# Performance work log

Hardware: AMD Instinct MI355X
Metric: run time of the kernel (lower is better)

## Reference

```python
import jax, jax.numpy as jnp
import numpy as np

N_NODES = 50000
N_EDGES = 1600000
IN_FEAT = 128
OUT_FEAT = 128


def setup_inputs() -> dict:
    key = jax.random.key(0)
    k_x, k_w, k_v, k_r, k_c = jax.random.split(key, 5)
    X = jax.random.normal(k_x, (N_NODES, IN_FEAT), dtype=jnp.float32)
    # nn.Linear(in_feat, out_feat, bias=False) weight: [out_feat, in_feat]
    W = jax.random.normal(k_w, (OUT_FEAT, IN_FEAT), dtype=jnp.float32) * (1.0 / np.sqrt(IN_FEAT))
    # Sparse adjacency A in COO form: A[rows[e], cols[e]] = vals[e]
    A_vals = jax.random.uniform(k_v, (N_EDGES,), dtype=jnp.float32)
    A_rows = jax.random.randint(k_r, (N_EDGES,), 0, N_NODES, dtype=jnp.int32)
    A_cols = jax.random.randint(k_c, (N_EDGES,), 0, N_NODES, dtype=jnp.int32)
    return {"X": X, "W": W, "A_vals": A_vals, "A_rows": A_rows, "A_cols": A_cols}


def reference(X, W, A_vals, A_rows, A_cols):
    # H = linear(X) = X @ W.T  -> [N, out_feat]
    H = jnp.einsum("ni,oi->no", X, W)
    # out = A @ H via COO SpMM: gather source rows, scale by edge value,
    # scatter-add into destination rows.
    msgs = A_vals[:, None] * H[A_cols]            # [E, out_feat]
    out = jax.ops.segment_sum(msgs, A_rows, num_segments=N_NODES)
    return out
```

## Files before the change

kernel.cpp:

```cpp
#include <hip/hip_runtime.h>


constexpr int N_NODES = 50000;
constexpr int N_EDGES = 1600000;
constexpr int FEAT    = 128;

constexpr int ROWS_PER_BIN = 64;
constexpr int NB           = (N_NODES + ROWS_PER_BIN - 1) / ROWS_PER_BIN;
constexpr int CAP          = 2560;
constexpr int CHUNK        = 4096;
constexpr int EPT          = 4;
constexpr int PART_BLOCKS  = (N_EDGES + CHUNK - 1) / CHUNK;
constexpr int GEMM_BLOCKS  = (N_NODES + 255) / 256;
constexpr int FUSED_GROUPS = 196;
constexpr int FUSED_BLOCKS = FUSED_GROUPS * 3;
constexpr int OVF_CAP      = 8192;

constexpr int RSLOT    = 64;
constexpr int ROVF_CAP = 256;

static_assert(NB % 2 == 0, "bin<->block mapping needs even NB");

constexpr int PITCH = 136;

typedef short short8 __attribute__((ext_vector_type(8)));
typedef float f32x4  __attribute__((ext_vector_type(4)));
typedef float f32x2  __attribute__((ext_vector_type(2)));

__device__ __forceinline__ unsigned short f2bf(float x) {
    unsigned u = __float_as_uint(x);
    u += 0x7fffu + ((u >> 16) & 1u);
    return (unsigned short)(u >> 16);
}
__device__ __forceinline__ float bf2f(unsigned short s) {
    return __uint_as_float(((unsigned)s) << 16);
}

__device__ __forceinline__ float dec_val10(unsigned w) {
    return (float)(w & 1023u) * (1.0f / 1023.0f);
}

__device__ void gemm_body(const float* __restrict__ X, const float* __restrict__ W,
                          unsigned short* __restrict__ Hb, int g,
                          unsigned short* Wsh) {
    const int tid  = threadIdx.x;
    const int row0 = g * 256;

#pragma unroll
    for (int t = 0; t < 4; t++) {
        int idx = tid + 1024 * t;
        int r   = idx >> 5;
        int c4  = (idx & 31) << 2;
        const float4 v = *(const float4*)&W[r * FEAT + c4];
        unsigned lo = f2bf(v.x) | ((unsigned)f2bf(v.y) << 16);
        unsigned hi = f2bf(v.z) | ((unsigned)f2bf(v.w) << 16);
        *(uint2*)&Wsh[r * PITCH + c4] = make_uint2(lo, hi);
    }
    __syncthreads();

    const int w    = tid >> 6;
    const int lane = tid & 63;
    const int n    = lane & 15;
    const int q    = lane >> 4;

    f32x4 acc[8];
#pragma unroll
    for (int t = 0; t < 8; t++) acc[t] = (f32x4){0.f, 0.f, 0.f, 0.f};

    int xrow = row0 + 16 * w + n;
    if (xrow >= N_NODES) xrow = N_NODES - 1;
    const float* xp = X + (size_t)xrow * FEAT;

#pragma unroll
    for (int kt = 0; kt < 4; kt++) {
        const int ko = kt * 32 + q * 8;
        const float4 a0 = *(const float4*)&xp[ko];
        const float4 a1 = *(const float4*)&xp[ko + 4];
        short8 bfrag;
        bfrag[0] = (short)f2bf(a0.x); bfrag[1] = (short)f2bf(a0.y);
        bfrag[2] = (short)f2bf(a0.z); bfrag[3] = (short)f2bf(a0.w);
        bfrag[4] = (short)f2bf(a1.x); bfrag[5] = (short)f2bf(a1.y);
        bfrag[6] = (short)f2bf(a1.z); bfrag[7] = (short)f2bf(a1.w);
#pragma unroll
        for (int t = 0; t < 8; t++) {
            const short8 afrag = *(const short8*)&Wsh[(16 * t + n) * PITCH + ko];
            acc[t] = __builtin_amdgcn_mfma_f32_16x16x32_bf16(afrag, bfrag, acc[t], 0, 0, 0);
        }
    }

    const int grow = row0 + 16 * w + n;
    if (grow < N_NODES) {
#pragma unroll
        for (int t = 0; t < 8; t++) {
            ushort4 pk;
            pk.x = f2bf(acc[t][0]); pk.y = f2bf(acc[t][1]);
            pk.z = f2bf(acc[t][2]); pk.w = f2bf(acc[t][3]);
            const int col0 = 16 * t + 4 * q;
            unsigned short* dst = Hb + ((size_t)(col0 >> 5) * N_NODES + grow) * 32
                                     + (col0 & 31);
            *(ushort4*)dst = pk;
        }
    }
}

__device__ void partition_body(const int* __restrict__ rows, const int* __restrict__ cols,
                               const float* __restrict__ vals,
                               int* __restrict__ gcur, unsigned* __restrict__ binbuf,
                               int* __restrict__ ovf_cnt, int* __restrict__ ovf,
                               int g, int* smem) {
    int* hist  = smem;
    int* wbase = smem + NB;
    const int tid = threadIdx.x;
    const int e0  = g * CHUNK;

    for (int i = tid; i < NB; i += 1024) hist[i] = 0;
    __syncthreads();

    int      myrow[EPT], myrank[EPT];
    unsigned myword[EPT];
#pragma unroll
    for (int t = 0; t < EPT; t++) {
        int e = e0 + t * 1024 + tid;
        if (e < N_EDGES) {
            int r = rows[e];
            unsigned vq = (unsigned)__float2int_rn(vals[e] * 1023.0f);
            myrow[t]  = r;
            myword[t] = ((unsigned)(r & 63) << 26) | ((unsigned)cols[e] << 10) | vq;
            myrank[t] = atomicAdd(&hist[r >> 6], 1);
        } else {
            myrow[t] = -1; myword[t] = 0; myrank[t] = 0;
        }
    }
    __syncthreads();

    for (int i = tid; i < NB; i += 1024) {
        int c = hist[i];
        wbase[i] = (c > 0) ? atomicAdd(&gcur[i], c) : 0;
    }
    __syncthreads();

#pragma unroll
    for (int t = 0; t < EPT; t++) {
        int r = myrow[t];
        if (r < 0) continue;
        int b    = r >> 6;
        int rank = wbase[b] + myrank[t];
        if (rank < CAP) {
            binbuf[(size_t)b * CAP + rank] = myword[t];
        } else {
            int k = atomicAdd(ovf_cnt, 1);
            if (k < OVF_CAP) ovf[k] = e0 + t * 1024 + tid;
        }
    }
}

__global__ __launch_bounds__(1024) void gemm_partition(
    const float* __restrict__ X, const float* __restrict__ W,
    unsigned short* __restrict__ Hb,
    const int* __restrict__ rows, const int* __restrict__ cols,
    const float* __restrict__ vals,
    int* __restrict__ gcur, unsigned* __restrict__ binbuf,
    int* __restrict__ ovf_cnt, int* __restrict__ ovf) {
    __shared__ unsigned short Wsh[128 * PITCH];
    const int grp = blockIdx.x / 3;
    const int rem = blockIdx.x - grp * 3;
    if (rem == 2) {
        gemm_body(X, W, Hb, grp, Wsh);
    } else {
        int pg = grp * 2 + rem;
        if (pg < PART_BLOCKS)
            partition_body(rows, cols, vals, gcur, binbuf, ovf_cnt, ovf, pg, (int*)Wsh);
    }
}

__global__ __launch_bounds__(512) void spmm_bins(
    const int* __restrict__ gcur, const unsigned* __restrict__ binbuf,
    const unsigned short* __restrict__ Hb, float* __restrict__ out,
    const int* __restrict__ rows, const int* __restrict__ cols,
    const float* __restrict__ vals,
    const int* __restrict__ ovf_cnt, const int* __restrict__ ovf) {
    __shared__ unsigned sorted[ROWS_PER_BIN * RSLOT];
    __shared__ int cur[ROWS_PER_BIN];
    __shared__ unsigned rovf[ROVF_CAP];
    __shared__ int rovf_cnt;

    const int bid  = blockIdx.x;
    const int q    = (bid & 7) >> 1;
    const int b    = (bid >> 3) * 2 + (bid & 1);
    const int tid  = threadIdx.x;
    const int lane = tid & 63;
    const int w    = tid >> 6;

    if (tid < ROWS_PER_BIN) cur[tid] = 0;
    if (tid == ROWS_PER_BIN) rovf_cnt = 0;
    __syncthreads();

    int cnt = gcur[b];
    if (cnt > CAP) cnt = CAP;
    const unsigned* bb = binbuf + (size_t)b * CAP;

    for (int i = tid; i < cnt; i += 512) {
        unsigned m   = bb[i];
        int rl       = (int)(m >> 26);
        int pos      = atomicAdd(&cur[rl], 1);
        unsigned col = (m >> 10) & 0xffffu;
        unsigned vb  = (unsigned)f2bf(dec_val10(m));
        if (pos < RSLOT) {
            sorted[rl * RSLOT + pos] = (vb << 16) | col;
        } else {
            int k = atomicAdd(&rovf_cnt, 1);
            if (k < ROVF_CAP) rovf[k] = m;
        }
    }
    __syncthreads();

    int nrovf = rovf_cnt;
    if (nrovf > ROVF_CAP) nrovf = ROVF_CAP;
    int novf = *ovf_cnt;
    if (novf > OVF_CAP) novf = OVF_CAP;

    const int row0   = b * ROWS_PER_BIN;
    const int slot   = lane >> 4;
    const int lane16 = lane & 15;
    const ushort2* __restrict__ Hq2 = (const ushort2*)(Hb + (size_t)q * N_NODES * 32);
    float2* out2 = (float2*)out;

    for (int rr = 0; rr < 8; rr++) {
        const int rl = w * 8 + rr;
        const int gr = row0 + rl;
        if (gr >= N_NODES) break;
        int e = cur[rl];
        if (e > RSLOT) e = RSLOT;
        const unsigned* srow = &sorted[rl * RSLOT];

        float accx = 0.f, accy = 0.f;
        int i = 0;
        for (; i + 16 <= e; i += 16) {
            float   vv[4];
            ushort2 hh[4];
#pragma unroll
            for (int u = 0; u < 4; u++) {
                unsigned m = srow[i + u * 4 + slot];
                vv[u] = __uint_as_float(m & 0xffff0000u);
                hh[u] = Hq2[(int)(m & 0xffffu) * 16 + lane16];
            }
#pragma unroll
            for (int u = 0; u < 4; u++) {
                accx += vv[u] * bf2f(hh[u].x);
                accy += vv[u] * bf2f(hh[u].y);
            }
        }
        for (; i < e; i += 4) {
            int idx = i + slot;
            unsigned m = (idx < e) ? srow[idx] : 0u;
            float v2 = __uint_as_float(m & 0xffff0000u);
            ushort2 h2 = Hq2[(int)(m & 0xffffu) * 16 + lane16];
            accx += v2 * bf2f(h2.x);
            accy += v2 * bf2f(h2.y);
        }
        for (int k = 0; k < nrovf; k++) {
            unsigned m = rovf[k];
            if ((int)(m >> 26) == rl && slot == 0) {
                float vv = dec_val10(m);
                ushort2 h2 = Hq2[(int)((m >> 10) & 0xffffu) * 16 + lane16];
                accx += vv * bf2f(h2.x);
                accy += vv * bf2f(h2.y);
            }
        }
        for (int k = 0; k < novf; k++) {
            int e2 = ovf[k];
            if (rows[e2] == gr && slot == 0) {
                float vv = vals[e2];
                ushort2 h2 = Hq2[cols[e2] * 16 + lane16];
                accx += vv * bf2f(h2.x);
                accy += vv * bf2f(h2.y);
            }
        }
        accx += __shfl_xor(accx, 16); accy += __shfl_xor(accy, 16);
        accx += __shfl_xor(accx, 32); accy += __shfl_xor(accy, 32);
        if (slot == 0) {
            f32x2 r; r[0] = accx; r[1] = accy;
            __builtin_nontemporal_store(r, (f32x2*)&out2[(size_t)gr * 64 + q * 16 + lane16]);
        }
    }
}

__global__ __launch_bounds__(1024) void gemm_only(
    const float* __restrict__ X, const float* __restrict__ W,
    unsigned short* __restrict__ Hb) {
    __shared__ unsigned short Wsh[128 * PITCH];
    gemm_body(X, W, Hb, blockIdx.x, Wsh);
}

__global__ __launch_bounds__(256) void spmm_push_atomic(
    const int* __restrict__ rows, const int* __restrict__ cols,
    const float* __restrict__ vals, const unsigned short* __restrict__ Hb,
    float* __restrict__ out) {
    const int e    = blockIdx.x * 4 + (threadIdx.x >> 6);
    const int lane = threadIdx.x & 63;
    if (e >= N_EDGES) return;
    int r = rows[e], c = cols[e];
    float v = vals[e];
    const int f1 = lane, f2 = lane + 64;
    float h1 = bf2f(Hb[((size_t)(f1 >> 5) * N_NODES + c) * 32 + (f1 & 31)]);
    float h2 = bf2f(Hb[((size_t)(f2 >> 5) * N_NODES + c) * 32 + (f2 & 31)]);
    atomicAdd(&out[r * FEAT + f1], v * h1);
    atomicAdd(&out[r * FEAT + f2], v * h2);
}

extern "C" void kernel_launch(void* const* d_in, const int* in_sizes, int n_in,
                              void* d_out, int out_size, void* d_ws, size_t ws_size,
                              hipStream_t stream) {
    const float* X      = (const float*)d_in[0];
    const float* W      = (const float*)d_in[1];
    const float* A_vals = (const float*)d_in[2];
    const int*   A_rows = (const int*)d_in[3];
    const int*   A_cols = (const int*)d_in[4];
    float* out = (float*)d_out;

    auto align256 = [](size_t x) { return (x + 255) & ~size_t(255); };
    char* ws = (char*)d_ws;

    size_t off = 0;
    size_t hb_off   = off; off += align256(size_t(N_NODES) * FEAT * 2);
    size_t gcur_off = off; off += align256(size_t(NB) * sizeof(int));
    size_t ovfc_off = off; off += 256;
    size_t ovf_off  = off; off += align256(size_t(OVF_CAP) * sizeof(int));
    size_t bin_off  = off; off += size_t(NB) * CAP * sizeof(unsigned);
    const size_t need = off;

    unsigned short* Hb = (unsigned short*)(ws + hb_off);

    if (ws_size >= need) {
        int*      gcur    = (int*)(ws + gcur_off);
        int*      ovf_cnt = (int*)(ws + ovfc_off);
        int*      ovf     = (int*)(ws + ovf_off);
        unsigned* binbuf  = (unsigned*)(ws + bin_off);

        (void)hipMemsetAsync(ws + gcur_off, 0, (ovfc_off - gcur_off) + 256, stream);
        gemm_partition<<<FUSED_BLOCKS, 1024, 0, stream>>>(X, W, Hb, A_rows, A_cols, A_vals,
                                                          gcur, binbuf, ovf_cnt, ovf);
        spmm_bins<<<NB * 4, 512, 0, stream>>>(gcur, binbuf, Hb, out,
                                              A_rows, A_cols, A_vals, ovf_cnt, ovf);
    } else {
        gemm_only<<<GEMM_BLOCKS, 1024, 0, stream>>>(X, W, Hb);
        (void)hipMemsetAsync(out, 0, size_t(N_NODES) * FEAT * sizeof(float), stream);
        spmm_push_atomic<<<(N_EDGES + 3) / 4, 256, 0, stream>>>(A_rows, A_cols, A_vals, Hb, out);
    }
}
```

Measured before the change: 164.2 us.

## Replace bin partitioning with per-row slot buckets and row-wise SpMM gather

```diff
diff --git a/kernel.cpp b/kernel.cpp
--- a/kernel.cpp
+++ b/kernel.cpp
@@ -16,6 +16,7 @@
 constexpr int FUSED_BLOCKS = FUSED_GROUPS * 3;
 constexpr int OVF_CAP      = 8192;
 
+constexpr int RSLOT_G  = 64;
 constexpr int RSLOT    = 64;
 constexpr int ROVF_CAP = 256;
 
@@ -35,7 +36,6 @@
 __device__ __forceinline__ float bf2f(unsigned short s) {
     return __uint_as_float(((unsigned)s) << 16);
 }
-
 __device__ __forceinline__ float dec_val10(unsigned w) {
     return (float)(w & 1023u) * (1.0f / 1023.0f);
 }
@@ -99,6 +99,121 @@
             unsigned short* dst = Hb + ((size_t)(col0 >> 5) * N_NODES + grow) * 32
                                      + (col0 & 31);
             *(ushort4*)dst = pk;
+        }
+    }
+}
+
+__device__ void partition_v2_body(const int* __restrict__ rows, const int* __restrict__ cols,
+                                  const float* __restrict__ vals,
+                                  int* __restrict__ rowcnt, unsigned* __restrict__ rowbuf,
+                                  int* __restrict__ ovf_cnt, int* __restrict__ ovf, int g) {
+    const int tid = threadIdx.x;
+    const int e0  = g * CHUNK;
+#pragma unroll
+    for (int t = 0; t < EPT; t++) {
+        int e = e0 + t * 1024 + tid;
+        if (e >= N_EDGES) continue;
+        int r = rows[e];
+        int c = cols[e];
+        int vq = __float2int_rn(vals[e] * 1023.0f);
+        unsigned vb = (unsigned)f2bf((float)vq * (1.0f / 1023.0f));
+        int pos = atomicAdd(&rowcnt[r], 1);
+        if (pos < RSLOT_G) {
+            rowbuf[(size_t)r * RSLOT_G + pos] = (vb << 16) | (unsigned)c;
+        } else {
+            int k = atomicAdd(ovf_cnt, 1);
+            if (k < OVF_CAP) ovf[k] = e;
+        }
+    }
+}
+
+__global__ __launch_bounds__(1024) void gemm_partition_v2(
+    const float* __restrict__ X, const float* __restrict__ W,
+    unsigned short* __restrict__ Hb,
+    const int* __restrict__ rows, const int* __restrict__ cols,
+    const float* __restrict__ vals,
+    int* __restrict__ rowcnt, unsigned* __restrict__ rowbuf,
+    int* __restrict__ ovf_cnt, int* __restrict__ ovf) {
+    __shared__ unsigned short Wsh[128 * PITCH];
+    const int grp = blockIdx.x / 3;
+    const int rem = blockIdx.x - grp * 3;
+    if (rem == 2) {
+        gemm_body(X, W, Hb, grp, Wsh);
+    } else {
+        int pg = grp * 2 + rem;
+        if (pg < PART_BLOCKS)
+            partition_v2_body(rows, cols, vals, rowcnt, rowbuf, ovf_cnt, ovf, pg);
+    }
+}
+
+__global__ __launch_bounds__(512) void spmm_rows(
+    const int* __restrict__ rowcnt, const unsigned* __restrict__ rowbuf,
+    const unsigned short* __restrict__ Hb, float* __restrict__ out,
+    const int* __restrict__ rows, const int* __restrict__ cols,
+    const float* __restrict__ vals,
+    const int* __restrict__ ovf_cnt, const int* __restrict__ ovf) {
+    const int bid  = blockIdx.x;
+    const int q    = (bid & 7) >> 1;
+    const int b    = (bid >> 3) * 2 + (bid & 1);
+    const int tid  = threadIdx.x;
+    const int lane = tid & 63;
+    const int w    = tid >> 6;
+
+    const int slot   = lane >> 4;
+    const int lane16 = lane & 15;
+    const ushort2* __restrict__ Hq2 = (const ushort2*)(Hb + (size_t)q * N_NODES * 32);
+    float2* out2 = (float2*)out;
+
+    int novf = *ovf_cnt;
+    if (novf > OVF_CAP) novf = OVF_CAP;
+
+    const int row0 = b * ROWS_PER_BIN;
+    for (int rr = 0; rr < 8; rr++) {
+        const int gr = row0 + w * 8 + rr;
+        if (gr >= N_NODES) break;
+        int e = rowcnt[gr];
+        if (e > RSLOT_G) e = RSLOT_G;
+        const unsigned* __restrict__ srow = rowbuf + (size_t)gr * RSLOT_G;
+
+        float accx = 0.f, accy = 0.f;
+        int i = 0;
+        for (; i + 16 <= e; i += 16) {
+            float   vv[4];
+            ushort2 hh[4];
+#pragma unroll
+            for (int u = 0; u < 4; u++) {
+                unsigned m = srow[i + u * 4 + slot];
+                vv[u] = __uint_as_float(m & 0xffff0000u);
+                hh[u] = Hq2[(int)(m & 0xffffu) * 16 + lane16];
+            }
+#pragma unroll
+            for (int u = 0; u < 4; u++) {
+                accx += vv[u] * bf2f(hh[u].x);
+                accy += vv[u] * bf2f(hh[u].y);
+            }
+        }
+        for (; i < e; i += 4) {
+            int idx = i + slot;
+            unsigned m = (idx < e) ? srow[idx] : 0u;
+            float v2 = __uint_as_float(m & 0xffff0000u);
+            ushort2 h2 = Hq2[(int)(m & 0xffffu) * 16 + lane16];
+            accx += v2 * bf2f(h2.x);
+            accy += v2 * bf2f(h2.y);
+        }
+        for (int k = 0; k < novf; k++) {
+            int e2 = ovf[k];
+            if (rows[e2] == gr && slot == 0) {
+                float vv = vals[e2];
+                ushort2 h2 = Hq2[cols[e2] * 16 + lane16];
+                accx += vv * bf2f(h2.x);
+                accy += vv * bf2f(h2.y);
+            }
+        }
+        accx += __shfl_xor(accx, 16); accy += __shfl_xor(accy, 16);
+        accx += __shfl_xor(accx, 32); accy += __shfl_xor(accy, 32);
+        if (slot == 0) {
+            f32x2 r; r[0] = accx; r[1] = accy;
+            __builtin_nontemporal_store(r, (f32x2*)&out2[(size_t)gr * 64 + q * 16 + lane16]);
         }
     }
 }
@@ -323,21 +438,39 @@
 
     size_t off = 0;
     size_t hb_off   = off; off += align256(size_t(N_NODES) * FEAT * 2);
-    size_t gcur_off = off; off += align256(size_t(NB) * sizeof(int));
+    size_t rc_off   = off; off += align256(size_t(N_NODES) * sizeof(int));
     size_t ovfc_off = off; off += 256;
     size_t ovf_off  = off; off += align256(size_t(OVF_CAP) * sizeof(int));
-    size_t bin_off  = off; off += size_t(NB) * CAP * sizeof(unsigned);
-    const size_t need = off;
+    size_t rb_off   = off; off += size_t(N_NODES) * RSLOT_G * sizeof(unsigned);
+    const size_t need_new = off;
+
+    size_t o2 = hb_off + align256(size_t(N_NODES) * FEAT * 2);
+    size_t gcur_off  = o2; o2 += align256(size_t(NB) * sizeof(int));
+    size_t ovfc2_off = o2; o2 += 256;
+    size_t ovf2_off  = o2; o2 += align256(size_t(OVF_CAP) * sizeof(int));
+    size_t bin_off   = o2; o2 += size_t(NB) * CAP * sizeof(unsigned);
+    const size_t need_old = o2;
 
     unsigned short* Hb = (unsigned short*)(ws + hb_off);
 
-    if (ws_size >= need) {
-        int*      gcur    = (int*)(ws + gcur_off);
+    if (ws_size >= need_new) {
+        int*      rowcnt  = (int*)(ws + rc_off);
         int*      ovf_cnt = (int*)(ws + ovfc_off);
         int*      ovf     = (int*)(ws + ovf_off);
+        unsigned* rowbuf  = (unsigned*)(ws + rb_off);
+
+        (void)hipMemsetAsync(ws + rc_off, 0, (ovfc_off - rc_off) + 256, stream);
+        gemm_partition_v2<<<FUSED_BLOCKS, 1024, 0, stream>>>(X, W, Hb, A_rows, A_cols, A_vals,
+                                                             rowcnt, rowbuf, ovf_cnt, ovf);
+        spmm_rows<<<NB * 4, 512, 0, stream>>>(rowcnt, rowbuf, Hb, out,
+                                              A_rows, A_cols, A_vals, ovf_cnt, ovf);
+    } else if (ws_size >= need_old) {
+        int*      gcur    = (int*)(ws + gcur_off);
+        int*      ovf_cnt = (int*)(ws + ovfc2_off);
+        int*      ovf     = (int*)(ws + ovf2_off);
         unsigned* binbuf  = (unsigned*)(ws + bin_off);
 
-        (void)hipMemsetAsync(ws + gcur_off, 0, (ovfc_off - gcur_off) + 256, stream);
+        (void)hipMemsetAsync(ws + gcur_off, 0, (ovfc2_off - gcur_off) + 256, stream);
         gemm_partition<<<FUSED_BLOCKS, 1024, 0, stream>>>(X, W, Hb, A_rows, A_cols, A_vals,
                                                           gcur, binbuf, ovf_cnt, ovf);
         spmm_bins<<<NB * 4, 512, 0, stream>>>(gcur, binbuf, Hb, out,
```

Result: slower. 256.0 us (+55.9%).

## Sort bins once in a separate kernel instead of per-quarter in SpMM

Applied to the files above, without the earlier changes.

```diff
diff --git a/kernel.cpp b/kernel.cpp
--- a/kernel.cpp
+++ b/kernel.cpp
@@ -16,8 +16,9 @@
 constexpr int FUSED_BLOCKS = FUSED_GROUPS * 3;
 constexpr int OVF_CAP      = 8192;
 
-constexpr int RSLOT    = 64;
-constexpr int ROVF_CAP = 256;
+constexpr int RSLOT     = 64;
+constexpr int GROVF_CAP = 4096;
+constexpr int ROVF_CAP  = 256;
 
 static_assert(NB % 2 == 0, "bin<->block mapping needs even NB");
 
@@ -35,7 +36,6 @@
 __device__ __forceinline__ float bf2f(unsigned short s) {
     return __uint_as_float(((unsigned)s) << 16);
 }
-
 __device__ __forceinline__ float dec_val10(unsigned w) {
     return (float)(w & 1023u) * (1.0f / 1023.0f);
 }
@@ -173,6 +173,145 @@
     }
 }
 
+__global__ __launch_bounds__(512) void sort_bins(
+    const int* __restrict__ gcur, const unsigned* __restrict__ binbuf,
+    unsigned* __restrict__ rowseg, int* __restrict__ rowcnt,
+    int* __restrict__ grovf_cnt, uint2* __restrict__ grovf) {
+    __shared__ unsigned slots[ROWS_PER_BIN * RSLOT];
+    __shared__ int cur[ROWS_PER_BIN];
+    const int b   = blockIdx.x;
+    const int tid = threadIdx.x;
+
+    if (tid < ROWS_PER_BIN) cur[tid] = 0;
+    __syncthreads();
+
+    int cnt = gcur[b];
+    if (cnt > CAP) cnt = CAP;
+    const unsigned* bb = binbuf + (size_t)b * CAP;
+
+    for (int i = tid; i < cnt; i += 512) {
+        unsigned m   = bb[i];
+        int rl       = (int)(m >> 26);
+        int pos      = atomicAdd(&cur[rl], 1);
+        unsigned col = (m >> 10) & 0xffffu;
+        unsigned vb  = (unsigned)f2bf(dec_val10(m));
+        unsigned wd  = (vb << 16) | col;
+        if (pos < RSLOT) {
+            slots[rl * RSLOT + pos] = wd;
+        } else {
+            int k = atomicAdd(grovf_cnt, 1);
+            if (k < GROVF_CAP) grovf[k] = make_uint2((unsigned)(b * 64 + rl), wd);
+        }
+    }
+    __syncthreads();
+
+    if (tid < ROWS_PER_BIN) {
+        int c = cur[tid];
+        rowcnt[b * 64 + tid] = (c < RSLOT) ? c : RSLOT;
+    }
+    uint4* dst = (uint4*)(rowseg + (size_t)b * (ROWS_PER_BIN * RSLOT));
+    const uint4* src = (const uint4*)slots;
+    for (int i = tid; i < ROWS_PER_BIN * RSLOT / 4; i += 512)
+        dst[i] = src[i];
+}
+
+__global__ __launch_bounds__(512) void spmm_quarters(
+    const unsigned* __restrict__ rowseg, const int* __restrict__ rowcnt,
+    const unsigned short* __restrict__ Hb, float* __restrict__ out,
+    const int* __restrict__ rows, const int* __restrict__ cols,
+    const float* __restrict__ vals,
+    const int* __restrict__ ovf_cnt, const int* __restrict__ ovf,
+    const int* __restrict__ grovf_cnt, const uint2* __restrict__ grovf) {
+    __shared__ unsigned seg[ROWS_PER_BIN * RSLOT];
+    __shared__ int cnt[ROWS_PER_BIN];
+
+    const int bid  = blockIdx.x;
+    const int q    = (bid & 7) >> 1;
+    const int b    = (bid >> 3) * 2 + (bid & 1);
+    const int tid  = threadIdx.x;
+    const int lane = tid & 63;
+    const int w    = tid >> 6;
+
+    {
+        uint4* d = (uint4*)seg;
+        const uint4* s = (const uint4*)(rowseg + (size_t)b * (ROWS_PER_BIN * RSLOT));
+#pragma unroll
+        for (int t = 0; t < 2; t++)
+            d[tid + 512 * t] = s[tid + 512 * t];
+    }
+    if (tid < ROWS_PER_BIN) cnt[tid] = rowcnt[b * 64 + tid];
+    __syncthreads();
+
+    int novf = *ovf_cnt;  if (novf > OVF_CAP)  novf = OVF_CAP;
+    int ngr  = *grovf_cnt; if (ngr > GROVF_CAP) ngr = GROVF_CAP;
+
+    const int eslot = lane >> 3;
+    const int lane8 = lane & 7;
+    const ushort4* __restrict__ Hq4 = (const ushort4*)(Hb + (size_t)q * N_NODES * 32);
+    const int row0 = b * ROWS_PER_BIN;
+
+    for (int rr = 0; rr < 8; rr++) {
+        const int rl = w * 8 + rr;
+        const int gr = row0 + rl;
+        if (gr >= N_NODES) break;
+        const int e = cnt[rl];
+        const unsigned* srow = &seg[rl * RSLOT];
+
+        float a0 = 0.f, a1 = 0.f, a2 = 0.f, a3 = 0.f;
+        int i = 0;
+        for (; i + 16 <= e; i += 16) {
+            unsigned m0 = srow[i + eslot];
+            unsigned m1 = srow[i + 8 + eslot];
+            float   v0 = __uint_as_float(m0 & 0xffff0000u);
+            float   v1 = __uint_as_float(m1 & 0xffff0000u);
+            ushort4 h0 = Hq4[(int)(m0 & 0xffffu) * 8 + lane8];
+            ushort4 h1 = Hq4[(int)(m1 & 0xffffu) * 8 + lane8];
+            a0 += v0 * bf2f(h0.x); a1 += v0 * bf2f(h0.y);
+            a2 += v0 * bf2f(h0.z); a3 += v0 * bf2f(h0.w);
+            a0 += v1 * bf2f(h1.x); a1 += v1 * bf2f(h1.y);
+            a2 += v1 * bf2f(h1.z); a3 += v1 * bf2f(h1.w);
+        }
+        for (; i < e; i += 8) {
+            int idx = i + eslot;
+            unsigned m = (idx < e) ? srow[idx] : 0u;
+            float v = __uint_as_float(m & 0xffff0000u);
+            ushort4 h = Hq4[(int)(m & 0xffffu) * 8 + lane8];
+            a0 += v * bf2f(h.x); a1 += v * bf2f(h.y);
+            a2 += v * bf2f(h.z); a3 += v * bf2f(h.w);
+        }
+        for (int k = 0; k < ngr; k++) {
+            uint2 gw = grovf[k];
+            if ((int)gw.x == gr && eslot == 0) {
+                unsigned m = gw.y;
+                float v = __uint_as_float(m & 0xffff0000u);
+                ushort4 h = Hq4[(int)(m & 0xffffu) * 8 + lane8];
+                a0 += v * bf2f(h.x); a1 += v * bf2f(h.y);
+                a2 += v * bf2f(h.z); a3 += v * bf2f(h.w);
+            }
+        }
+        for (int k = 0; k < novf; k++) {
+            int e2 = ovf[k];
+            if (rows[e2] == gr && eslot == 0) {
+                float v = vals[e2];
+                ushort4 h = Hq4[cols[e2] * 8 + lane8];
+                a0 += v * bf2f(h.x); a1 += v * bf2f(h.y);
+                a2 += v * bf2f(h.z); a3 += v * bf2f(h.w);
+            }
+        }
+        a0 += __shfl_xor(a0, 8);  a1 += __shfl_xor(a1, 8);
+        a2 += __shfl_xor(a2, 8);  a3 += __shfl_xor(a3, 8);
+        a0 += __shfl_xor(a0, 16); a1 += __shfl_xor(a1, 16);
+        a2 += __shfl_xor(a2, 16); a3 += __shfl_xor(a3, 16);
+        a0 += __shfl_xor(a0, 32); a1 += __shfl_xor(a1, 32);
+        a2 += __shfl_xor(a2, 32); a3 += __shfl_xor(a3, 32);
+        if (eslot == 0) {
+            f32x4 r; r[0] = a0; r[1] = a1; r[2] = a2; r[3] = a3;
+            __builtin_nontemporal_store(r,
+                (f32x4*)&out[(size_t)gr * FEAT + q * 32 + lane8 * 4]);
+        }
+    }
+}
+
 __global__ __launch_bounds__(512) void spmm_bins(
     const int* __restrict__ gcur, const unsigned* __restrict__ binbuf,
     const unsigned short* __restrict__ Hb, float* __restrict__ out,
@@ -327,11 +466,32 @@
     size_t ovfc_off = off; off += 256;
     size_t ovf_off  = off; off += align256(size_t(OVF_CAP) * sizeof(int));
     size_t bin_off  = off; off += size_t(NB) * CAP * sizeof(unsigned);
-    const size_t need = off;
+    const size_t need_old = off;
+    size_t rseg_off = off; off += size_t(NB) * ROWS_PER_BIN * RSLOT * 4;
+    size_t rcnt_off = off; off += align256(size_t(NB) * ROWS_PER_BIN * 4);
+    size_t grov_off = off; off += size_t(GROVF_CAP) * sizeof(uint2);
+    const size_t need_new = off;
 
     unsigned short* Hb = (unsigned short*)(ws + hb_off);
 
-    if (ws_size >= need) {
+    if (ws_size >= need_new) {
+        int*      gcur      = (int*)(ws + gcur_off);
+        int*      ovf_cnt   = (int*)(ws + ovfc_off);
+        int*      grovf_cnt = (int*)(ws + ovfc_off + 64);
+        int*      ovf       = (int*)(ws + ovf_off);
+        unsigned* binbuf    = (unsigned*)(ws + bin_off);
+        unsigned* rowseg    = (unsigned*)(ws + rseg_off);
+        int*      rowcnt    = (int*)(ws + rcnt_off);
+        uint2*    grovf     = (uint2*)(ws + grov_off);
+
+        (void)hipMemsetAsync(ws + gcur_off, 0, (ovfc_off - gcur_off) + 256, stream);
+        gemm_partition<<<FUSED_BLOCKS, 1024, 0, stream>>>(X, W, Hb, A_rows, A_cols, A_vals,
+                                                          gcur, binbuf, ovf_cnt, ovf);
+        sort_bins<<<NB, 512, 0, stream>>>(gcur, binbuf, rowseg, rowcnt, grovf_cnt, grovf);
+        spmm_quarters<<<NB * 4, 512, 0, stream>>>(rowseg, rowcnt, Hb, out,
+                                                  A_rows, A_cols, A_vals,
+                                                  ovf_cnt, ovf, grovf_cnt, grovf);
+    } else if (ws_size >= need_old) {
         int*      gcur    = (int*)(ws + gcur_off);
         int*      ovf_cnt = (int*)(ws + ovfc_off);
         int*      ovf     = (int*)(ws + ovf_off);
```

Measured after the change: 177.7 us. 8.2% more time.
